# Kernel optimization log

Measured on AMD Instinct MI355X. Metric: run time of the kernel, lower is better.

Reference implementation:

```python
import jax, jax.numpy as jnp
import numpy as np

NUM_LEVELS = 4
RADIUS = 4


def _avg_pool2(x):
    # x: [B,S,C,H,W] -> 2x2 average pool, stride 2
    B, S, C, H, W = x.shape
    return x.reshape(B, S, C, H // 2, 2, W // 2, 2).mean(axis=(4, 6))


def _bilinear_sample(corr, x, y):
    # corr: [B,S,N,H,W]; x,y: [B,S,N,K,K] pixel coords; zeros padding, align_corners=True
    B, S, N, H, W = corr.shape
    corr_flat = corr.reshape(B, S, N, H * W)
    x0f = jnp.floor(x)
    y0f = jnp.floor(y)
    x0 = x0f.astype(jnp.int32)
    y0 = y0f.astype(jnp.int32)
    x1 = x0 + 1
    y1 = y0 + 1
    wx1 = x - x0f
    wx0 = 1.0 - wx1
    wy1 = y - y0f
    wy0 = 1.0 - wy1

    def gather(ix, iy):
        valid = ((ix >= 0) & (ix < W) & (iy >= 0) & (iy < H)).astype(corr.dtype)
        idx = jnp.clip(iy, 0, H - 1) * W + jnp.clip(ix, 0, W - 1)
        flat_idx = idx.reshape(B, S, N, -1)
        v = jnp.take_along_axis(corr_flat, flat_idx, axis=-1).reshape(ix.shape)
        return v * valid

    return (gather(x0, y0) * wx0 * wy0 + gather(x1, y0) * wx1 * wy0 +
            gather(x0, y1) * wx0 * wy1 + gather(x1, y1) * wx1 * wy1)


def _forward(features, targets, coordinates):
    B, S, C, H, W = features.shape
    N = targets.shape[2]
    inv_sqrt_c = 1.0 / jnp.sqrt(jnp.asarray(C, jnp.float32))

    # build feature pyramid
    pyramid = [features]
    f = features
    for _ in range(NUM_LEVELS - 1):
        f = _avg_pool2(f)
        pyramid.append(f)

    # correlate + windowed sample per level
    K = 2 * RADIUS + 1
    d = jnp.linspace(-RADIUS, RADIUS, K, dtype=jnp.float32)
    # faithful to torch: stack(meshgrid(dy, dx, indexing='ij'), -1)
    dyy, dxx = jnp.meshgrid(d, d, indexing='ij')
    delta = jnp.stack([dyy, dxx], axis=-1)  # [K,K,2]

    out_pyramid = []
    for i, feats in enumerate(pyramid):
        _, _, _, Hi, Wi = feats.shape
        # correlation volume [B,S,N,Hi,Wi]
        corr = jnp.einsum('bsnc,bschw->bsnhw', targets, feats) * inv_sqrt_c
        # window centers at this level
        centroid = coordinates[:, :, :, None, None, :] / (2.0 ** i)  # [B,S,N,1,1,2]
        pts = centroid + delta  # [B,S,N,K,K,2]; [...,0]=x, [...,1]=y (split order in torch code)
        sampled = _bilinear_sample(corr, pts[..., 0], pts[..., 1])  # [B,S,N,K,K]
        out_pyramid.append(sampled.reshape(B, S, N, K * K))

    return jnp.concatenate(out_pyramid, axis=-1)  # [B,S,N,NUM_LEVELS*K*K]


def setup_inputs() -> dict:
    key = jax.random.key(0)
    k1, k2, k3 = jax.random.split(key, 3)
    B, S, C, H, W = 1, 2, 128, 64, 96
    N = H * W
    features = jax.random.normal(k1, (B, S, C, H, W), dtype=jnp.float32)
    targets = jax.random.normal(k2, (B, S, N, C), dtype=jnp.float32)
    u = jax.random.uniform(k3, (B, S, N, 2), dtype=jnp.float32)
    scale = jnp.asarray([W - 1, H - 1], jnp.float32)  # x in [0,W-1], y in [0,H-1]
    coordinates = u * scale
    return {"features": features, "targets": targets, "coordinates": coordinates}


def reference(features, targets, coordinates):
    return _forward(features, targets, coordinates)
```

## Files before the change

kernel.cpp:

```cpp
#include <hip/hip_runtime.h>
#include <hip/hip_bf16.h>

#define SDIM 2
#define NPT  6144
#define CDIM 128
#define H0   64
#define W0   96

typedef __fp16 half2_t __attribute__((ext_vector_type(2)));

__constant__ int c_lvl_off[4] = {0, 786432, 983040, 1032192};

__device__ __forceinline__ unsigned pack_f16(float a, float b) {
    half2_t h = __builtin_amdgcn_cvt_pkrtz(a, b);
    return __builtin_bit_cast(unsigned, h);
}

__device__ __forceinline__ half2_t as_h2(unsigned u) {
    return __builtin_bit_cast(half2_t, u);
}

__global__ __launch_bounds__(256) void transpose_kernel(const float* __restrict__ feat,
                                                        unsigned* __restrict__ out) {
    __shared__ float lds[64 * 129];
    const int bid = blockIdx.x;
    const int s = bid / 96;
    const int p0 = (bid % 96) * 64;
    const int tid = threadIdx.x;
    const int sub = tid >> 6;
    const int lane = tid & 63;
#pragma unroll
    for (int k = 0; k < 32; ++k) {
        int c = sub + k * 4;
        lds[lane * 129 + c] = feat[(s * CDIM + c) * (H0 * W0) + p0 + lane];
    }
    __syncthreads();
#pragma unroll
    for (int k = 0; k < 16; ++k) {
        int pl = sub + k * 4;
        float lo = lds[pl * 129 + lane * 2];
        float hi = lds[pl * 129 + lane * 2 + 1];
        out[(size_t)(s * (H0 * W0) + p0 + pl) * 64 + lane] = pack_f16(lo, hi);
    }
}

__global__ __launch_bounds__(256) void pool_all_kernel(const unsigned* __restrict__ pyr0,
                                                       unsigned* __restrict__ pyr) {
    int idx = blockIdx.x * 256 + threadIdx.x;
    int lvl, rem;
    if (idx < 196608)      { lvl = 1; rem = idx; }
    else if (idx < 245760) { lvl = 2; rem = idx - 196608; }
    else if (idx < 258048) { lvl = 3; rem = idx - 245760; }
    else return;

    const int m = 1 << lvl;
    const int Wi = W0 >> lvl;
    const int Hi = H0 >> lvl;
    const int cp = rem & 63;
    const int pix = rem >> 6;
    const int x = pix % Wi;
    const int t = pix / Wi;
    const int y = t % Hi;
    const int s = t / Hi;

    const int row_stride = W0 * 64;
    const unsigned* base = pyr0 + ((s * H0 + y * m) * W0 + x * m) * 64 + cp;

    float lo = 0.0f, hi = 0.0f;
    for (int dy = 0; dy < m; ++dy) {
        const unsigned* rp = base + dy * row_stride;
        for (int dx = 0; dx < m; ++dx) {
            half2_t v = as_h2(rp[dx * 64]);
            lo += (float)v.x;
            hi += (float)v.y;
        }
    }
    const float inv = 1.0f / (float)(m * m);
    pyr[c_lvl_off[lvl] + rem] = pack_f16(lo * inv, hi * inv);
}

__global__ __launch_bounds__(256) void corr_kernel(const float* __restrict__ targets,
                                                   const float* __restrict__ coords,
                                                   const unsigned* __restrict__ pyr,
                                                   float* __restrict__ out) {
    __shared__ __align__(16) float tgt[CDIM];
    __shared__ float Ds[4][112];

    const int sn = blockIdx.x;
    const int tid = threadIdx.x;

    if (tid < CDIM) tgt[tid] = targets[(size_t)sn * CDIM + tid];
    const float cx = coords[sn * 2 + 0];
    const float cy = coords[sn * 2 + 1];
    __syncthreads();

    const int lvl = tid >> 6;
    const int lane = tid & 63;
    const int g = lane >> 2;
    const int k = lane & 3;

    const int Wi = W0 >> lvl;
    const int Hi = H0 >> lvl;
    const int s = sn / NPT;
    const unsigned* base = pyr + c_lvl_off[lvl] + s * Hi * Wi * 64;

    const float scale = 1.0f / (float)(1 << lvl);
    const float cxl = cx * scale, cyl = cy * scale;
    const float x0f = floorf(cxl), y0f = floorf(cyl);
    const float wx1 = cxl - x0f, wx0 = 1.0f - wx1;
    const float wy1 = cyl - y0f, wy0 = 1.0f - wy1;
    const int ix0 = (int)x0f - 4;
    const int iy0 = (int)y0f - 4;

    half2_t treg[16];
#pragma unroll
    for (int q = 0; q < 16; ++q)
        treg[q] = __builtin_amdgcn_cvt_pkrtz(tgt[k * 32 + 2 * q], tgt[k * 32 + 2 * q + 1]);

    for (int it = 0; it < 7; ++it) {
        int p = it * 16 + g;
        if (p < 100) {
            int row = (p * 205) >> 11;
            int col = p - row * 10;
            int y = iy0 + row;
            int x = ix0 + col;
            bool valid = ((unsigned)x < (unsigned)Wi) && ((unsigned)y < (unsigned)Hi);
            int xc = min(max(x, 0), Wi - 1);
            int yc = min(max(y, 0), Hi - 1);
            const uint4* ptr = (const uint4*)(base + (yc * Wi + xc) * 64 + k * 16);
            float acc0 = 0.0f, acc1 = 0.0f;
#pragma unroll
            for (int q = 0; q < 4; ++q) {
                uint4 v = ptr[q];
                acc0 = __builtin_amdgcn_fdot2(as_h2(v.x), treg[q * 4 + 0], acc0, false);
                acc1 = __builtin_amdgcn_fdot2(as_h2(v.y), treg[q * 4 + 1], acc1, false);
                acc0 = __builtin_amdgcn_fdot2(as_h2(v.z), treg[q * 4 + 2], acc0, false);
                acc1 = __builtin_amdgcn_fdot2(as_h2(v.w), treg[q * 4 + 3], acc1, false);
            }
            float acc = acc0 + acc1;
            acc += __shfl_xor(acc, 1);
            acc += __shfl_xor(acc, 2);
            if (k == 0) Ds[lvl][p] = valid ? acc : 0.0f;
        }
    }

    __syncthreads();

    const float isc = 0.08838834764831843f;
    const size_t obase = (size_t)sn * 324 + lvl * 81;
#pragma unroll
    for (int r = 0; r < 2; ++r) {
        int o = r * 64 + lane;
        if (o < 81) {
            int j = (o * 57) >> 9;
            int i = o - j * 9;
            float d00 = Ds[lvl][i * 10 + j];
            float d01 = Ds[lvl][i * 10 + j + 1];
            float d10 = Ds[lvl][(i + 1) * 10 + j];
            float d11 = Ds[lvl][(i + 1) * 10 + j + 1];
            float v = wy0 * (wx0 * d00 + wx1 * d01) + wy1 * (wx0 * d10 + wx1 * d11);
            out[obase + o] = v * isc;
        }
    }
}

extern "C" void kernel_launch(void* const* d_in, const int* in_sizes, int n_in,
                              void* d_out, int out_size, void* d_ws, size_t ws_size,
                              hipStream_t stream) {
    const float* features = (const float*)d_in[0];
    const float* targets  = (const float*)d_in[1];
    const float* coords   = (const float*)d_in[2];
    float* out = (float*)d_out;

    unsigned* pyr = (unsigned*)d_ws;

    transpose_kernel<<<SDIM * (H0 * W0 / 64), 256, 0, stream>>>(features, pyr);

    pool_all_kernel<<<(258048 + 255) / 256, 256, 0, stream>>>(pyr, pyr);

    corr_kernel<<<SDIM * NPT, 256, 0, stream>>>(targets, coords, pyr, out);
}
```

Before: 163.2 us.

## Prefetch next pyramid gather in corr kernel and drop LDS target staging

The correlation kernel now software-pipelines its gathers. It issues the four 16-byte loads for the next window pixel before computing the dot products for the current one, and it fully unrolls the 7-iteration loop. Targets are read straight from global memory as float4 and packed to fp16 in registers, which removes the LDS staging and the first block barrier. The second __syncthreads is replaced by an LDS waitcnt, since each level's samples are written and read by the same wavefront. The aim is to hide gather latency and cut barrier overhead, at the cost of more registers and a few redundant clamped loads past pixel 100.

Result: slower. 204.7 us (+25.4%).

```diff
diff --git a/kernel.cpp b/kernel.cpp
--- a/kernel.cpp
+++ b/kernel.cpp
@@ -83,17 +83,10 @@
                                                    const float* __restrict__ coords,
                                                    const unsigned* __restrict__ pyr,
                                                    float* __restrict__ out) {
-    __shared__ __align__(16) float tgt[CDIM];
     __shared__ float Ds[4][112];
 
     const int sn = blockIdx.x;
     const int tid = threadIdx.x;
-
-    if (tid < CDIM) tgt[tid] = targets[(size_t)sn * CDIM + tid];
-    const float cx = coords[sn * 2 + 0];
-    const float cy = coords[sn * 2 + 1];
-    __syncthreads();
-
     const int lvl = tid >> 6;
     const int lane = tid & 63;
     const int g = lane >> 2;
@@ -104,6 +97,8 @@
     const int s = sn / NPT;
     const unsigned* base = pyr + c_lvl_off[lvl] + s * Hi * Wi * 64;
 
+    const float cx = coords[sn * 2 + 0];
+    const float cy = coords[sn * 2 + 1];
     const float scale = 1.0f / (float)(1 << lvl);
     const float cxl = cx * scale, cyl = cy * scale;
     const float x0f = floorf(cxl), y0f = floorf(cyl);
@@ -113,38 +108,67 @@
     const int iy0 = (int)y0f - 4;
 
     half2_t treg[16];
-#pragma unroll
-    for (int q = 0; q < 16; ++q)
-        treg[q] = __builtin_amdgcn_cvt_pkrtz(tgt[k * 32 + 2 * q], tgt[k * 32 + 2 * q + 1]);
-
+    const float4* tp = (const float4*)(targets + (size_t)sn * CDIM + k * 32);
+#pragma unroll
+    for (int q = 0; q < 8; ++q) {
+        float4 v = tp[q];
+        treg[2 * q + 0] = __builtin_amdgcn_cvt_pkrtz(v.x, v.y);
+        treg[2 * q + 1] = __builtin_amdgcn_cvt_pkrtz(v.z, v.w);
+    }
+
+    auto paddr = [&](int p) -> const uint4* {
+        int row = (p * 205) >> 11;
+        int col = p - row * 10;
+        int xc = min(max(ix0 + col, 0), Wi - 1);
+        int yc = min(max(iy0 + row, 0), Hi - 1);
+        return (const uint4*)(base + (yc * Wi + xc) * 64 + k * 16);
+    };
+
+    uint4 buf0, buf1, buf2, buf3;
+    {
+        const uint4* ptr = paddr(g);
+        buf0 = ptr[0]; buf1 = ptr[1]; buf2 = ptr[2]; buf3 = ptr[3];
+    }
+
+#pragma unroll
     for (int it = 0; it < 7; ++it) {
-        int p = it * 16 + g;
-        if (p < 100) {
+        const int p = it * 16 + g;
+        uint4 n0, n1, n2, n3;
+        if (it < 6) {
+            const uint4* nptr = paddr(p + 16);
+            n0 = nptr[0]; n1 = nptr[1]; n2 = nptr[2]; n3 = nptr[3];
+        }
+        float acc0 = 0.0f, acc1 = 0.0f;
+        acc0 = __builtin_amdgcn_fdot2(as_h2(buf0.x), treg[0],  acc0, false);
+        acc1 = __builtin_amdgcn_fdot2(as_h2(buf0.y), treg[1],  acc1, false);
+        acc0 = __builtin_amdgcn_fdot2(as_h2(buf0.z), treg[2],  acc0, false);
+        acc1 = __builtin_amdgcn_fdot2(as_h2(buf0.w), treg[3],  acc1, false);
+        acc0 = __builtin_amdgcn_fdot2(as_h2(buf1.x), treg[4],  acc0, false);
+        acc1 = __builtin_amdgcn_fdot2(as_h2(buf1.y), treg[5],  acc1, false);
+        acc0 = __builtin_amdgcn_fdot2(as_h2(buf1.z), treg[6],  acc0, false);
+        acc1 = __builtin_amdgcn_fdot2(as_h2(buf1.w), treg[7],  acc1, false);
+        acc0 = __builtin_amdgcn_fdot2(as_h2(buf2.x), treg[8],  acc0, false);
+        acc1 = __builtin_amdgcn_fdot2(as_h2(buf2.y), treg[9],  acc1, false);
+        acc0 = __builtin_amdgcn_fdot2(as_h2(buf2.z), treg[10], acc0, false);
+        acc1 = __builtin_amdgcn_fdot2(as_h2(buf2.w), treg[11], acc1, false);
+        acc0 = __builtin_amdgcn_fdot2(as_h2(buf3.x), treg[12], acc0, false);
+        acc1 = __builtin_amdgcn_fdot2(as_h2(buf3.y), treg[13], acc1, false);
+        acc0 = __builtin_amdgcn_fdot2(as_h2(buf3.z), treg[14], acc0, false);
+        acc1 = __builtin_amdgcn_fdot2(as_h2(buf3.w), treg[15], acc1, false);
+        float acc = acc0 + acc1;
+        acc += __shfl_xor(acc, 1);
+        acc += __shfl_xor(acc, 2);
+        if (k == 0 && p < 100) {
             int row = (p * 205) >> 11;
             int col = p - row * 10;
-            int y = iy0 + row;
-            int x = ix0 + col;
+            int x = ix0 + col, y = iy0 + row;
             bool valid = ((unsigned)x < (unsigned)Wi) && ((unsigned)y < (unsigned)Hi);
-            int xc = min(max(x, 0), Wi - 1);
-            int yc = min(max(y, 0), Hi - 1);
-            const uint4* ptr = (const uint4*)(base + (yc * Wi + xc) * 64 + k * 16);
-            float acc0 = 0.0f, acc1 = 0.0f;
-#pragma unroll
-            for (int q = 0; q < 4; ++q) {
-                uint4 v = ptr[q];
-                acc0 = __builtin_amdgcn_fdot2(as_h2(v.x), treg[q * 4 + 0], acc0, false);
-                acc1 = __builtin_amdgcn_fdot2(as_h2(v.y), treg[q * 4 + 1], acc1, false);
-                acc0 = __builtin_amdgcn_fdot2(as_h2(v.z), treg[q * 4 + 2], acc0, false);
-                acc1 = __builtin_amdgcn_fdot2(as_h2(v.w), treg[q * 4 + 3], acc1, false);
-            }
-            float acc = acc0 + acc1;
-            acc += __shfl_xor(acc, 1);
-            acc += __shfl_xor(acc, 2);
-            if (k == 0) Ds[lvl][p] = valid ? acc : 0.0f;
-        }
-    }
-
-    __syncthreads();
+            Ds[lvl][p] = valid ? acc : 0.0f;
+        }
+        if (it < 6) { buf0 = n0; buf1 = n1; buf2 = n2; buf3 = n3; }
+    }
+
+    asm volatile("s_waitcnt lgkmcnt(0)" ::: "memory");
 
     const float isc = 0.08838834764831843f;
     const size_t obase = (size_t)sn * 324 + lvl * 81;
```
